# Kernel optimization log

Hardware: AMD Instinct MI355X
Metric: run time of the kernel (lower is better)

## Reference

```python
import jax, jax.numpy as jnp
import numpy as np

TEMPORAL_WIDTH = 4  # hardcoded in GRUBlock


def causal_conv1d(x, w, b):
    """Depthwise causal temporal conv. x:[B,T,R], w:[4,R], b:[R].
    out[t] = sum_i w[i] * x[t - 3 + i] + b (zero left padding)."""
    T = x.shape[1]
    xp = jnp.pad(x, ((0, 0), (TEMPORAL_WIDTH - 1, 0), (0, 0)))
    y = b
    for i in range(TEMPORAL_WIDTH):  # tiny fixed loop over 4 taps
        y = y + w[i] * xp[:, i:i + T]
    return y


def linear_scan(a, b):
    """h_t = a_t * h_{t-1} + b_t with h_{-1}=0, via associative scan over time."""
    def comb(e1, e2):
        a1, b1 = e1
        a2, b2 = e2
        return a2 * a1, a2 * b1 + b2
    _, h = jax.lax.associative_scan(comb, (a, b), axis=1)
    return h


def setup_inputs() -> dict:
    key = jax.random.key(0)
    k1, k2, k3, k4 = jax.random.split(key, 4)
    B, T, H, R = 4, 8192, 1024, 1024
    x = jax.random.normal(k1, (B, T, H), dtype=jnp.float32)
    # lecun init: N(0, 1/sqrt(d_in)); torch Linear weight is [out, in]
    w_zh = jax.random.normal(k2, (2 * R, H), dtype=jnp.float32) / np.sqrt(H)
    w_out = jax.random.normal(k3, (H, R), dtype=jnp.float32) / np.sqrt(R)
    conv_w = jax.random.normal(k4, (TEMPORAL_WIDTH, R), dtype=jnp.float32) / np.sqrt(TEMPORAL_WIDTH)
    conv_b = jnp.zeros((R,), dtype=jnp.float32)
    return {"x": x, "w_zh": w_zh, "w_out": w_out, "conv_w": conv_w, "conv_b": conv_b}


def reference(x, w_zh, w_out, conv_w, conv_b):
    # residual causal conv
    x = x + causal_conv1d(x, conv_w, conv_b)
    # fused z/h projection: [B,T,H] @ [H,2R]
    zh = jnp.einsum('bth,rh->btr', x, w_zh)
    z, h = jnp.split(zh, 2, axis=-1)
    z = jax.nn.sigmoid(z)
    # GRU-style linear recurrence: h_t = (1-z_t) h_{t-1} + z_t h~_t
    h_o = linear_scan(1.0 - z, z * h)
    return jnp.einsum('btr,hr->bth', h_o, w_out)
```

## Files before the change

kernel.cpp:

```cpp
#include <hip/hip_runtime.h>

typedef __bf16 bf16x8 __attribute__((ext_vector_type(8)));
typedef __bf16 bf16x4 __attribute__((ext_vector_type(4)));
typedef float  f32x4  __attribute__((ext_vector_type(4)));

static constexpr int Bb = 4, T = 8192, H = 1024, R = 1024;
static constexpr int BT = Bb * T;
static constexpr int N1 = 2 * R;
static constexpr int CH = 64;
static constexpr int L  = T / CH;

__device__ __forceinline__ void g2lds16(const void* g, void* l) {
  __builtin_amdgcn_global_load_lds(
      (const __attribute__((address_space(1))) unsigned int*)g,
      (__attribute__((address_space(3))) unsigned int*)l, 16, 0, 0);
}

__global__ __launch_bounds__(256) void cast_f32_bf16(const float* __restrict__ in,
                                                     __bf16* __restrict__ out, int n4) {
  int i = blockIdx.x * 256 + threadIdx.x;
  if (i >= n4) return;
  const f32x4 v = *(const f32x4*)(in + (size_t)i * 4);
  bf16x4 o;
  o[0] = (__bf16)v[0]; o[1] = (__bf16)v[1]; o[2] = (__bf16)v[2]; o[3] = (__bf16)v[3];
  *(bf16x4*)(out + (size_t)i * 4) = o;
}

__global__ __launch_bounds__(256) void conv_residual_cast(const float* __restrict__ x,
                                                          const float* __restrict__ cw,
                                                          const float* __restrict__ cb,
                                                          __bf16* __restrict__ xc) {
  const size_t i4 = (size_t)blockIdx.x * 256 + threadIdx.x;
  const size_t v  = i4 * 4;
  const int    h  = (int)(v & (size_t)(H - 1));
  const size_t bt = v >> 10;
  const int    t  = (int)(bt & (size_t)(T - 1));
  f32x4 acc = *(const f32x4*)(cb + h);
  const f32x4 xv = *(const f32x4*)(x + v);
#pragma unroll
  for (int i = 0; i < 4; ++i) {
    const int tt = t - 3 + i;
    if (tt >= 0) {
      const f32x4 xi = *(const f32x4*)(x + (bt - 3 + i) * H + h);
      const f32x4 wi = *(const f32x4*)(cw + i * H + h);
      acc += wi * xi;
    }
  }
  acc += xv;
  bf16x4 o;
  o[0] = (__bf16)acc[0]; o[1] = (__bf16)acc[1]; o[2] = (__bf16)acc[2]; o[3] = (__bf16)acc[3];
  *(bf16x4*)(xc + v) = o;
}


#define STG_A(buf, k0, ro) g2lds16(aBase + (size_t)(r + (ro)) * K + (k0), \
                                   &sA[buf][(w8 + (ro)) * 64])
#define STG_B(buf, k0, ro) g2lds16(bBase + (size_t)(rB + (ro)) * K + (k0), \
                                   &sB[buf][(w8B + (ro)) * 64])
#define STAGE_A02(buf, kt) do { const int k0_ = (kt) * 64; STG_A(buf, k0_, 0);  STG_A(buf, k0_, 128); } while (0)
#define STAGE_A13(buf, kt) do { const int k0_ = (kt) * 64; STG_A(buf, k0_, 64); STG_A(buf, k0_, 192); } while (0)
#define STAGE_BEV(buf, kt) do { const int k0_ = (kt) * 64; STG_B(buf, k0_, 0);  STG_B(buf, k0_, 128); } while (0)
#define STAGE_BOD(buf, kt) do { const int k0_ = (kt) * 64; STG_B(buf, k0_, 32); STG_B(buf, k0_, 160); } while (0)

#define RD_A(dst, MQ) do {                                                           \
    _Pragma("unroll") for (int i_ = 0; i_ < 4; ++i_) {                               \
      const int rt_ = aRowBase + (MQ) * 64 + i_ * 16;                                \
      _Pragma("unroll") for (int ks_ = 0; ks_ < 2; ++ks_)                            \
        dst[i_][ks_] = *(const bf16x8*)&sAc[rt_ * 64 + (((ks_ * 4 + kg) ^ (rt_ & 7)) * 8)]; \
    } } while (0)

#define RD_B(dst, NQ) do {                                                           \
    _Pragma("unroll") for (int j_ = 0; j_ < 2; ++j_) {                               \
      const int rt_ = bRowBase + (NQ) * 32 + j_ * 16;                                \
      _Pragma("unroll") for (int ks_ = 0; ks_ < 2; ++ks_)                            \
        dst[j_][ks_] = *(const bf16x8*)&sBc[rt_ * 64 + (((ks_ * 4 + kg) ^ (rt_ & 7)) * 8)]; \
    } } while (0)

#define MMA(AF, BF, MQ, NQ) do {                                                     \
    asm volatile("s_barrier" ::: "memory");                                          \
    asm volatile("s_waitcnt lgkmcnt(0)" ::: "memory");                               \
    __builtin_amdgcn_s_setprio(1);                                                   \
    _Pragma("unroll") for (int i_ = 0; i_ < 4; ++i_)                                 \
      _Pragma("unroll") for (int j_ = 0; j_ < 2; ++j_)                               \
        _Pragma("unroll") for (int ks_ = 0; ks_ < 2; ++ks_)                          \
          acc[(MQ) * 4 + i_][(NQ) * 2 + j_] = __builtin_amdgcn_mfma_f32_16x16x32_bf16( \
              AF[i_][ks_], BF[j_][ks_], acc[(MQ) * 4 + i_][(NQ) * 2 + j_], 0, 0, 0); \
    __builtin_amdgcn_s_setprio(0);                                                   \
  } while (0)

template <typename OUT_T>
__global__ __launch_bounds__(512, 2) void gemm256(const __bf16* __restrict__ A,
                                                  const __bf16* __restrict__ Bm,
                                                  OUT_T* __restrict__ C,
                                                  int M, int N, int K, int nbx) {
  __shared__ __align__(16) __bf16 sA[2][256 * 64];
  __shared__ __align__(16) __bf16 sB[2][256 * 64];
  const int tid  = threadIdx.x;
  const int wave = tid >> 6;
  const int lane = tid & 63;
  const int wm = wave >> 2;
  const int wn = wave & 3;

  const int nwg = gridDim.x;
  int wg = blockIdx.x;
  wg = (wg & 7) * (nwg >> 3) + (wg >> 3);
  const int bm0 = (wg / nbx) * 256;
  const int bn0 = (wg % nbx) * 256;

  const int NT = K >> 6;

  const int r   = tid >> 3;
  const int sgc = (tid & 7) ^ (r & 7);
  const int rB  = r + (r & 32);
  const int w8  = wave * 8;
  const int w8B = w8 + (w8 & 32);
  const __bf16* aBase = A  + (size_t)bm0 * K + sgc * 8;
  const __bf16* bBase = Bm + (size_t)bn0 * K + sgc * 8;

  const int l15 = lane & 15;
  const int kg  = lane >> 4;
  const int aRowBase = wm * 128 + l15;
  const int bRowBase = wn * 64 + l15;

  f32x4 acc[8][4] = {};

  STAGE_BEV(0, 0);
  STAGE_A02(0, 0);
  STAGE_A13(0, 0);
  STAGE_BOD(0, 0);
  {
    const int k1 = NT > 1 ? 1 : 0;
    STAGE_BEV(1, k1);
    STAGE_A02(1, k1);
  }
  asm volatile("s_waitcnt vmcnt(4)" ::: "memory");
  asm volatile("s_barrier" ::: "memory");

  for (int kt = 0; kt < NT; ++kt) {
    const int cur = kt & 1, nxt = cur ^ 1;
    const int kt1 = (kt + 1 < NT) ? kt + 1 : NT - 1;
    const int kt2 = (kt + 2 < NT) ? kt + 2 : NT - 1;
    const __bf16* sAc = sA[cur];
    const __bf16* sBc = sB[cur];
    bf16x8 afA[4][2], afB[4][2], bfE[2][2], bfO[2][2];

    RD_A(afA, 0);
    RD_B(bfE, 0);
    STAGE_A13(nxt, kt1);
    asm volatile("s_waitcnt lgkmcnt(8)" ::: "memory");
    MMA(afA, bfE, 0, 0);
    asm volatile("s_barrier" ::: "memory");
    RD_B(bfO, 1);
    STAGE_BOD(nxt, kt1);
    MMA(afA, bfO, 0, 1);
    asm volatile("s_barrier" ::: "memory");
    RD_A(afB, 1);
    STAGE_BEV(cur, kt2);
    MMA(afB, bfO, 1, 1);
    asm volatile("s_barrier" ::: "memory");
    STAGE_A02(cur, kt2);
    MMA(afB, bfE, 1, 0);
    asm volatile("s_waitcnt vmcnt(4)" ::: "memory");
    asm volatile("s_barrier" ::: "memory");
  }

  const int orow0 = bm0 + wm * 128 + kg * 4;
  const int ocol0 = bn0 + wn * 64 + l15;
#pragma unroll
  for (int mi = 0; mi < 8; ++mi)
#pragma unroll
    for (int nj = 0; nj < 4; ++nj) {
      const size_t rbase = (size_t)(orow0 + mi * 16);
#pragma unroll
      for (int rr = 0; rr < 4; ++rr)
        C[(rbase + rr) * N + (ocol0 + nj * 16)] = (OUT_T)acc[mi][nj][rr];
    }
}

__global__ __launch_bounds__(256) void scan_pass1(const __bf16* __restrict__ zh,
                                                  float* __restrict__ aggA,
                                                  float* __restrict__ aggB) {
  const int r = (blockIdx.x * 256 + threadIdx.x) * 4;
  const int c = blockIdx.y;
  const int b = blockIdx.z;
  size_t base = ((size_t)b * T + (size_t)c * L) * N1 + r;
  float Aacc[4] = {1.f, 1.f, 1.f, 1.f};
  float Bacc[4] = {0.f, 0.f, 0.f, 0.f};
#pragma unroll 4
  for (int t = 0; t < L; ++t) {
    const bf16x4 s4 = *(const bf16x4*)(zh + base);
    const bf16x4 h4 = *(const bf16x4*)(zh + base + R);
    base += N1;
#pragma unroll
    for (int j = 0; j < 4; ++j) {
      const float z = 1.f / (1.f + __expf(-(float)s4[j]));
      const float a = 1.f - z;
      Bacc[j] = a * Bacc[j] + z * (float)h4[j];
      Aacc[j] *= a;
    }
  }
  const size_t o = ((size_t)b * CH + c) * R + r;
  *(f32x4*)(aggA + o) = f32x4{Aacc[0], Aacc[1], Aacc[2], Aacc[3]};
  *(f32x4*)(aggB + o) = f32x4{Bacc[0], Bacc[1], Bacc[2], Bacc[3]};
}

__global__ __launch_bounds__(256) void scan_pass2(const float* __restrict__ aggA,
                                                  const float* __restrict__ aggB,
                                                  float* __restrict__ carry) {
  const int idx = blockIdx.x * 256 + threadIdx.x;
  const int b = idx >> 10;
  const int r = idx & (R - 1);
  float h = 0.f;
#pragma unroll 8
  for (int c = 0; c < CH; ++c) {
    const size_t o = ((size_t)b * CH + c) * R + r;
    carry[o] = h;
    h = aggA[o] * h + aggB[o];
  }
}

__global__ __launch_bounds__(256) void scan_pass3(const __bf16* __restrict__ zh,
                                                  const float* __restrict__ carry,
                                                  __bf16* __restrict__ ho) {
  const int r = (blockIdx.x * 256 + threadIdx.x) * 4;
  const int c = blockIdx.y;
  const int b = blockIdx.z;
  size_t base  = ((size_t)b * T + (size_t)c * L) * N1 + r;
  size_t obase = ((size_t)b * T + (size_t)c * L) * R + r;
  float h[4];
  const f32x4 cv = *(const f32x4*)(carry + ((size_t)b * CH + c) * R + r);
  h[0] = cv[0]; h[1] = cv[1]; h[2] = cv[2]; h[3] = cv[3];
#pragma unroll 4
  for (int t = 0; t < L; ++t) {
    const bf16x4 s4 = *(const bf16x4*)(zh + base);
    const bf16x4 h4 = *(const bf16x4*)(zh + base + R);
    base += N1;
    bf16x4 o;
#pragma unroll
    for (int j = 0; j < 4; ++j) {
      const float z = 1.f / (1.f + __expf(-(float)s4[j]));
      h[j] = (1.f - z) * h[j] + z * (float)h4[j];
      o[j] = (__bf16)h[j];
    }
    *(bf16x4*)(ho + obase) = o;
    obase += R;
  }
}

extern "C" void kernel_launch(void* const* d_in, const int* in_sizes, int n_in,
                              void* d_out, int out_size, void* d_ws, size_t ws_size,
                              hipStream_t stream) {
  const float* x      = (const float*)d_in[0];
  const float* w_zh   = (const float*)d_in[1];
  const float* w_out  = (const float*)d_in[2];
  const float* conv_w = (const float*)d_in[3];
  const float* conv_b = (const float*)d_in[4];
  float* out = (float*)d_out;

  char* ws = (char*)d_ws;
  size_t off = 0;
  __bf16* wzh_b  = (__bf16*)(ws + off); off += (size_t)N1 * H * 2;
  __bf16* wout_b = (__bf16*)(ws + off); off += (size_t)H * R * 2;
  __bf16* xc     = (__bf16*)(ws + off); off += (size_t)BT * H * 2;
  __bf16* zh     = (__bf16*)(ws + off); off += (size_t)BT * N1 * 2;
  float*  aggA   = (float*)(ws + off);  off += (size_t)Bb * CH * R * 4;
  float*  aggB   = (float*)(ws + off);  off += (size_t)Bb * CH * R * 4;
  float*  carry  = (float*)(ws + off);  off += (size_t)Bb * CH * R * 4;
  __bf16* ho = xc;

  cast_f32_bf16<<<(N1 * H / 4 + 255) / 256, 256, 0, stream>>>(w_zh, wzh_b, N1 * H / 4);
  cast_f32_bf16<<<(H * R / 4 + 255) / 256, 256, 0, stream>>>(w_out, wout_b, H * R / 4);
  conv_residual_cast<<<BT * H / 4 / 256, 256, 0, stream>>>(x, conv_w, conv_b, xc);
  gemm256<__bf16><<<(BT / 256) * (N1 / 256), 512, 0, stream>>>(xc, wzh_b, zh, BT, N1, H, N1 / 256);
  scan_pass1<<<dim3(R / 4 / 256, CH, Bb), 256, 0, stream>>>(zh, aggA, aggB);
  scan_pass2<<<Bb * R / 256, 256, 0, stream>>>(aggA, aggB, carry);
  scan_pass3<<<dim3(R / 4 / 256, CH, Bb), 256, 0, stream>>>(zh, carry, ho);
  gemm256<float><<<(BT / 256) * (H / 256), 512, 0, stream>>>(ho, wout_b, out, BT, H, R, H / 256);
}
```

Measured before the change: 616.0 us.

## Prefetch next-tile LDS fragments across GEMM iterations and double scan chunks

Restructures the bf16 GEMM main loop so the A and B fragments for the next K-tile are read from LDS at the end of the current iteration. This lets those reads overlap the MFMA clusters, and the explicit lgkmcnt waits plus one barrier per MMA phase are dropped, with sched_barrier fences added to keep the ordering. The scan chunk count goes from 64 to 128, shortening each sequential chunk while enlarging the carry pass. The scan aggregates now reuse the w_zh bf16 buffer, which is dead after the first GEMM. The risk is that the relaxed synchronization and wait counts must still cover the reads of buffers being restaged, and holding the prefetched fragments raises register pressure.

New measurement: 568.8 us. 7.7% less time.

```diff
diff --git a/kernel.cpp b/kernel.cpp
--- a/kernel.cpp
+++ b/kernel.cpp
@@ -7,7 +7,7 @@
 static constexpr int Bb = 4, T = 8192, H = 1024, R = 1024;
 static constexpr int BT = Bb * T;
 static constexpr int N1 = 2 * R;
-static constexpr int CH = 64;
+static constexpr int CH = 128;
 static constexpr int L  = T / CH;
 
 __device__ __forceinline__ void g2lds16(const void* g, void* l) {
@@ -62,23 +62,21 @@
 #define STAGE_BEV(buf, kt) do { const int k0_ = (kt) * 64; STG_B(buf, k0_, 0);  STG_B(buf, k0_, 128); } while (0)
 #define STAGE_BOD(buf, kt) do { const int k0_ = (kt) * 64; STG_B(buf, k0_, 32); STG_B(buf, k0_, 160); } while (0)
 
-#define RD_A(dst, MQ) do {                                                           \
+#define RD_A(dst, MQ, SRC) do {                                                      \
     _Pragma("unroll") for (int i_ = 0; i_ < 4; ++i_) {                               \
       const int rt_ = aRowBase + (MQ) * 64 + i_ * 16;                                \
       _Pragma("unroll") for (int ks_ = 0; ks_ < 2; ++ks_)                            \
-        dst[i_][ks_] = *(const bf16x8*)&sAc[rt_ * 64 + (((ks_ * 4 + kg) ^ (rt_ & 7)) * 8)]; \
+        dst[i_][ks_] = *(const bf16x8*)&(SRC)[rt_ * 64 + (((ks_ * 4 + kg) ^ (rt_ & 7)) * 8)]; \
     } } while (0)
 
-#define RD_B(dst, NQ) do {                                                           \
+#define RD_B(dst, NQ, SRC) do {                                                      \
     _Pragma("unroll") for (int j_ = 0; j_ < 2; ++j_) {                               \
       const int rt_ = bRowBase + (NQ) * 32 + j_ * 16;                                \
       _Pragma("unroll") for (int ks_ = 0; ks_ < 2; ++ks_)                            \
-        dst[j_][ks_] = *(const bf16x8*)&sBc[rt_ * 64 + (((ks_ * 4 + kg) ^ (rt_ & 7)) * 8)]; \
+        dst[j_][ks_] = *(const bf16x8*)&(SRC)[rt_ * 64 + (((ks_ * 4 + kg) ^ (rt_ & 7)) * 8)]; \
     } } while (0)
 
-#define MMA(AF, BF, MQ, NQ) do {                                                     \
-    asm volatile("s_barrier" ::: "memory");                                          \
-    asm volatile("s_waitcnt lgkmcnt(0)" ::: "memory");                               \
+#define MFMA_CL(AF, BF, MQ, NQ) do {                                                 \
     __builtin_amdgcn_s_setprio(1);                                                   \
     _Pragma("unroll") for (int i_ = 0; i_ < 4; ++i_)                                 \
       _Pragma("unroll") for (int j_ = 0; j_ < 2; ++j_)                               \
@@ -87,6 +85,10 @@
               AF[i_][ks_], BF[j_][ks_], acc[(MQ) * 4 + i_][(NQ) * 2 + j_], 0, 0, 0); \
     __builtin_amdgcn_s_setprio(0);                                                   \
   } while (0)
+
+#define SB0 __builtin_amdgcn_sched_barrier(0)
+#define BARRIER asm volatile("s_barrier" ::: "memory")
+#define VMCNT4 asm volatile("s_waitcnt vmcnt(4)" ::: "memory")
 
 template <typename OUT_T>
 __global__ __launch_bounds__(512, 2) void gemm256(const __bf16* __restrict__ A,
@@ -123,6 +125,7 @@
   const int bRowBase = wn * 64 + l15;
 
   f32x4 acc[8][4] = {};
+  bf16x8 afA[4][2], afB[4][2], bfE[2][2], bfO[2][2];
 
   STAGE_BEV(0, 0);
   STAGE_A02(0, 0);
@@ -133,8 +136,10 @@
     STAGE_BEV(1, k1);
     STAGE_A02(1, k1);
   }
-  asm volatile("s_waitcnt vmcnt(4)" ::: "memory");
-  asm volatile("s_barrier" ::: "memory");
+  VMCNT4;
+  BARRIER;
+  RD_A(afA, 0, sA[0]);
+  RD_B(bfE, 0, sB[0]);
 
   for (int kt = 0; kt < NT; ++kt) {
     const int cur = kt & 1, nxt = cur ^ 1;
@@ -142,26 +147,32 @@
     const int kt2 = (kt + 2 < NT) ? kt + 2 : NT - 1;
     const __bf16* sAc = sA[cur];
     const __bf16* sBc = sB[cur];
-    bf16x8 afA[4][2], afB[4][2], bfE[2][2], bfO[2][2];
-
-    RD_A(afA, 0);
-    RD_B(bfE, 0);
+    const __bf16* sAn = sA[nxt];
+    const __bf16* sBn = sB[nxt];
+
+    RD_B(bfO, 1, sBc);
     STAGE_A13(nxt, kt1);
-    asm volatile("s_waitcnt lgkmcnt(8)" ::: "memory");
-    MMA(afA, bfE, 0, 0);
-    asm volatile("s_barrier" ::: "memory");
-    RD_B(bfO, 1);
+    SB0;
+    MFMA_CL(afA, bfE, 0, 0);
+    BARRIER;
+    RD_A(afB, 1, sAc);
     STAGE_BOD(nxt, kt1);
-    MMA(afA, bfO, 0, 1);
-    asm volatile("s_barrier" ::: "memory");
-    RD_A(afB, 1);
+    SB0;
+    MFMA_CL(afA, bfO, 0, 1);
+    VMCNT4;
+    BARRIER;
+    RD_A(afA, 0, sAn);
     STAGE_BEV(cur, kt2);
-    MMA(afB, bfO, 1, 1);
-    asm volatile("s_barrier" ::: "memory");
+    SB0;
+    MFMA_CL(afB, bfO, 1, 1);
+    BARRIER;
     STAGE_A02(cur, kt2);
-    MMA(afB, bfE, 1, 0);
-    asm volatile("s_waitcnt vmcnt(4)" ::: "memory");
-    asm volatile("s_barrier" ::: "memory");
+    SB0;
+    MFMA_CL(afB, bfE, 1, 0);
+    SB0;
+    RD_B(bfE, 0, sBn);
+    VMCNT4;
+    BARRIER;
   }
 
   const int orow0 = bm0 + wm * 128 + kg * 4;
@@ -263,9 +274,9 @@
   __bf16* wout_b = (__bf16*)(ws + off); off += (size_t)H * R * 2;
   __bf16* xc     = (__bf16*)(ws + off); off += (size_t)BT * H * 2;
   __bf16* zh     = (__bf16*)(ws + off); off += (size_t)BT * N1 * 2;
-  float*  aggA   = (float*)(ws + off);  off += (size_t)Bb * CH * R * 4;
-  float*  aggB   = (float*)(ws + off);  off += (size_t)Bb * CH * R * 4;
   float*  carry  = (float*)(ws + off);  off += (size_t)Bb * CH * R * 4;
+  float*  aggA   = (float*)wzh_b;
+  float*  aggB   = (float*)((char*)wzh_b + (size_t)Bb * CH * R * 4);
   __bf16* ho = xc;
 
   cast_f32_bf16<<<(N1 * H / 4 + 255) / 256, 256, 0, stream>>>(w_zh, wzh_b, N1 * H / 4);
```
